# Optimization experiments

Hardware: AMD Instinct MI355X
Metric: run time of the kernel (lower is better)

Reference implementation:

```python
import jax, jax.numpy as jnp
import numpy as np

P = 16        # patch_size
SP = 8        # shift_pixels = int(patch_size * shift_ratio)
EPS = 1e-5    # torch LayerNorm default eps


def _bilinear_shift(img, sx, sy):
    """Replicates F.grid_sample(bilinear, zeros padding, align_corners=False)
    with a pure translation grid: out[y, x] = img[y + sy, x + sx] (bilinear)."""
    B, C, H, W = img.shape
    ys = jnp.arange(H, dtype=img.dtype) + jnp.asarray(sy, img.dtype)
    xs = jnp.arange(W, dtype=img.dtype) + jnp.asarray(sx, img.dtype)
    y0 = jnp.floor(ys)
    x0 = jnp.floor(xs)
    wy = ys - y0  # [H]
    wx = xs - x0  # [W]

    def gather(iy, ix):
        valid = ((iy >= 0) & (iy < H))[:, None] & ((ix >= 0) & (ix < W))[None, :]
        iyc = jnp.clip(iy, 0, H - 1).astype(jnp.int32)
        ixc = jnp.clip(ix, 0, W - 1).astype(jnp.int32)
        v = img[:, :, iyc][:, :, :, ixc]  # [B, C, H, W]
        return v * valid.astype(img.dtype)

    w00 = (1 - wy)[:, None] * (1 - wx)[None, :]
    w01 = (1 - wy)[:, None] * wx[None, :]
    w10 = wy[:, None] * (1 - wx)[None, :]
    w11 = wy[:, None] * wx[None, :]
    return (w00 * gather(y0, x0) + w01 * gather(y0, x0 + 1)
            + w10 * gather(y0 + 1, x0) + w11 * gather(y0 + 1, x0 + 1))


def reference(x, ln_gamma, ln_beta, w, b):
    B, C, H, W = x.shape
    # Original bug: shift_y = (shift_x * 2 / W) * 2 / H, so the effective
    # vertical pixel shift is ty*H/2 = 2*SP/W (sign of shift_x; dy ignored).
    ty_pix = 2.0 * SP / W
    right_up = _bilinear_shift(x, +SP, +ty_pix)
    left_up = _bilinear_shift(x, -SP, -ty_pix)
    right_down = _bilinear_shift(x, +SP, +ty_pix)
    left_down = _bilinear_shift(x, -SP, -ty_pix)
    xc = jnp.concatenate([x, left_up, right_up, left_down, right_down], axis=1)  # [B, 5C, H, W]
    C5 = xc.shape[1]
    h, ww = H // P, W // P
    # Rearrange 'B C (p1 h) (p2 w) -> B (h w) (C p1 p2)'  (p1/p2 are OUTER factors)
    p = xc.reshape(B, C5, P, h, P, ww)
    p = p.transpose(0, 3, 5, 1, 2, 4).reshape(B, h * ww, C5 * P * P)  # [B, 196, 3840]
    # LayerNorm (biased variance, as in torch)
    mu = p.mean(axis=-1, keepdims=True)
    var = p.var(axis=-1, keepdims=True)
    p = (p - mu) * jax.lax.rsqrt(var + EPS) * ln_gamma + ln_beta
    # Linear
    return p @ w + b  # [B, 196, 768]


def setup_inputs() -> dict:
    key = jax.random.key(0)
    k1, k2 = jax.random.split(key)
    d_in = P * P * 5 * 3  # 3840
    d_model = 768
    return {
        "x": jax.random.normal(k1, (64, 3, 224, 224), dtype=jnp.float32),
        "ln_gamma": jnp.ones((d_in,), dtype=jnp.float32),
        "ln_beta": jnp.zeros((d_in,), dtype=jnp.float32),
        "w": jax.random.normal(k2, (d_in, d_model), dtype=jnp.float32) / np.sqrt(d_in),
        "b": jnp.zeros((d_model,), dtype=jnp.float32),
    }
```

## Files before the change

kernel.cpp:

```cpp
#include <hip/hip_runtime.h>


typedef short bf16x8 __attribute__((ext_vector_type(8)));
typedef unsigned short u16x8 __attribute__((ext_vector_type(8)));
typedef float f32x4 __attribute__((ext_vector_type(4)));

#define GLOBAL_AS __attribute__((address_space(1)))
#define LDS_AS __attribute__((address_space(3)))

__device__ __forceinline__ unsigned short f2bf(float f) {
  union { float f; unsigned int u; } v;
  v.f = f;
  unsigned int u = v.u;
  unsigned int r = (u + 0x7FFFu + ((u >> 16) & 1u)) >> 16;
  return (unsigned short)r;
}

__global__ __launch_bounds__(256) void spt_fold_w(
    const float* __restrict__ gamma, const float* __restrict__ beta,
    const float* __restrict__ w, unsigned short* __restrict__ w2t,
    float* __restrict__ Gp, float* __restrict__ Bp)
{
  __shared__ float tile[16][257];
  const int f2blk = blockIdx.x * 16;
  const int jblk  = blockIdx.y * 256;
  const int t = threadIdx.x;
  const int j = jblk + t;
  float gacc = 0.f, bacc = 0.f;
  #pragma unroll
  for (int i = 0; i < 16; ++i) {
    const int f2 = f2blk + i;
    const int g = f2 / 768;
    const int rem = f2 % 768;
    float v, bv;
    if (g == 0) {
      const int f = rem;
      const float wv = w[(size_t)f * 768 + j];
      v = gamma[f] * wv;
      bv = beta[f] * wv;
    } else if (g == 1) {
      const int fa = 768 + rem, fb = 2304 + rem;
      const float wa = w[(size_t)fa * 768 + j], wb = w[(size_t)fb * 768 + j];
      v = gamma[fa] * wa + gamma[fb] * wb;
      bv = beta[fa] * wa + beta[fb] * wb;
    } else {
      const int fa = 1536 + rem, fb = 3072 + rem;
      const float wa = w[(size_t)fa * 768 + j], wb = w[(size_t)fb * 768 + j];
      v = gamma[fa] * wa + gamma[fb] * wb;
      bv = beta[fa] * wa + beta[fb] * wb;
    }
    tile[i][t] = v;
    gacc += v;
    bacc += bv;
  }
  __syncthreads();
  u16x8 lo, hi;
  #pragma unroll
  for (int i = 0; i < 8; ++i) {
    lo[i] = f2bf(tile[i][t]);
    hi[i] = f2bf(tile[8 + i][t]);
  }
  unsigned short* dst = w2t + (size_t)j * 2304 + f2blk;
  *(u16x8*)dst = lo;
  *(u16x8*)(dst + 8) = hi;
  Gp[blockIdx.x * 768 + j] = gacc;
  Bp[blockIdx.x * 768 + j] = bacc;
}

__global__ __launch_bounds__(256) void spt_gb(
    const float* __restrict__ Gp, const float* __restrict__ Bp,
    const float* __restrict__ bvec, float* __restrict__ G, float* __restrict__ Bt)
{
  const int j = blockIdx.x * 256 + threadIdx.x;
  float g = 0.f, bb = 0.f;
  for (int i = 0; i < 144; ++i) {
    g += Gp[i * 768 + j];
    bb += Bp[i * 768 + j];
  }
  G[j] = g;
  Bt[j] = bb + bvec[j];
}

__global__ __launch_bounds__(256) void spt_pack(
    const float* __restrict__ x, unsigned short* __restrict__ V,
    float2* __restrict__ stats)
{
  __shared__ unsigned short slab[14 * 2312];
  __shared__ float sred[4][224];
  __shared__ float qred[4][224];
  const int bi = blockIdx.x;
  const int b = bi / 14, hi = bi % 14;
  const int t = threadIdx.x;
  const float TW = 16.0f / 224.0f;

  const int q = t % 56;
  const int grp = t / 56;
  const int x4 = q * 4;

  int sloff[4];
  {
    int wi = x4 % 14, p2 = x4 / 14;
    #pragma unroll
    for (int j = 0; j < 4; ++j) {
      sloff[j] = wi * 2312 + p2;
      if (++wi == 14) { wi = 0; ++p2; }
    }
  }

  if (t < 224) {
    f32x4 sAcc = {0.f, 0.f, 0.f, 0.f}, qAcc = {0.f, 0.f, 0.f, 0.f};
    #pragma unroll
    for (int it = 0; it < 12; ++it) {
      const int cp = grp * 12 + it;
      const int c = cp >> 4, p1 = cp & 15;
      const int y = p1 * 14 + hi;
      const float* row = x + ((size_t)(b * 3 + c)) * 50176 + (size_t)y * 224;
      const f32x4 xv = *(const f32x4*)(row + x4);
      f32x4 ra = {0.f,0.f,0.f,0.f}, rb = {0.f,0.f,0.f,0.f};
      f32x4 la = {0.f,0.f,0.f,0.f}, lb = {0.f,0.f,0.f,0.f};
      if (q < 54) {
        ra = *(const f32x4*)(row + x4 + 8);
        if (y < 223) rb = *(const f32x4*)(row + x4 + 8 + 224);
      }
      if (q >= 2) {
        la = *(const f32x4*)(row + x4 - 8);
        if (y > 0) lb = *(const f32x4*)(row + x4 - 8 - 224);
      }
      const f32x4 rv = (1.0f - TW) * ra + TW * rb;
      const f32x4 lv = (1.0f - TW) * la + TW * lb;
      sAcc += xv + 2.0f * (lv + rv);
      qAcc += xv * xv + 2.0f * (lv * lv + rv * rv);
      const int kb = c * 256 + p1 * 16;
      #pragma unroll
      for (int j = 0; j < 4; ++j) {
        slab[sloff[j] + kb]        = f2bf(xv[j]);
        slab[sloff[j] + kb + 768]  = f2bf(lv[j]);
        slab[sloff[j] + kb + 1536] = f2bf(rv[j]);
      }
    }
    #pragma unroll
    for (int j = 0; j < 4; ++j) {
      sred[grp][x4 + j] = sAcc[j];
      qred[grp][x4 + j] = qAcc[j];
    }
  }
  __syncthreads();

  float ss = 0.f, qq = 0.f;
  if (t < 224) {
    ss = sred[0][t] + sred[1][t] + sred[2][t] + sred[3][t];
    qq = qred[0][t] + qred[1][t] + qred[2][t] + qred[3][t];
  }
  __syncthreads();
  if (t < 224) { sred[0][t] = ss; qred[0][t] = qq; }
  __syncthreads();

  const int tok0 = b * 196 + hi * 14;
  if (t < 14) {
    float S = 0.f, Q = 0.f;
    #pragma unroll
    for (int p = 0; p < 16; ++p) { S += sred[0][t + 14 * p]; Q += qred[0][t + 14 * p]; }
    const float mu = S / 3840.f;
    const float var = Q / 3840.f - mu * mu;
    const float r = rsqrtf(var + 1e-5f);
    stats[tok0 + t] = make_float2(r, -mu * r);
  }

  if (t < 224) {
    const int wi2 = t >> 4, sub = t & 15;
    const size_t vbase = (size_t)(tok0 + wi2) * 2304;
    #pragma unroll
    for (int cc = 0; cc < 18; ++cc) {
      const int off8 = (cc * 16 + sub) * 8;
      *(u16x8*)&V[vbase + off8] = *(const u16x8*)&slab[wi2 * 2312 + off8];
    }
  }
}

__global__ __launch_bounds__(256, 2) void spt_gemm(
    const unsigned short* __restrict__ V, const unsigned short* __restrict__ w2t,
    const float2* __restrict__ stats, const float* __restrict__ G,
    const float* __restrict__ Bt, float* __restrict__ out)
{
  __shared__ unsigned short Alds[2][224 * 64];
  __shared__ unsigned short Blds[2][96 * 64];

  const int orig = blockIdx.x;
  const int wgid = (orig & 7) * 56 + (orig >> 3);
  const int m0 = (wgid >> 3) * 224;
  const int n0 = (wgid & 7) * 96;
  const int t = threadIdx.x;
  const int w = t >> 6, l = t & 63;
  const int wr = w >> 1;
  const int wn = w & 1;

  f32x4 acc[7][3] = {};

#define STAGE(pb, kt)                                                          \
  {                                                                            \
    const int k0s = (kt) << 6;                                                 \
    _Pragma("unroll") for (int i = 0; i < 7; ++i) {                            \
      const int c = i * 256 + t;                                               \
      const int row = c >> 3;                                                  \
      const int srcel = (((c & 7) ^ (row & 7)) << 3);                          \
      const unsigned short* ga = V + (size_t)(m0 + row) * 2304 + k0s + srcel;  \
      __builtin_amdgcn_global_load_lds((const GLOBAL_AS unsigned int*)ga,      \
          (LDS_AS unsigned int*)&Alds[pb][i * 2048 + w * 512], 16, 0, 0);      \
    }                                                                          \
    _Pragma("unroll") for (int i = 0; i < 3; ++i) {                            \
      const int c = i * 256 + t;                                               \
      const int row = c >> 3;                                                  \
      const int srcel = (((c & 7) ^ (row & 7)) << 3);                          \
      const unsigned short* gb = w2t + (size_t)(n0 + row) * 2304 + k0s + srcel;\
      __builtin_amdgcn_global_load_lds((const GLOBAL_AS unsigned int*)gb,      \
          (LDS_AS unsigned int*)&Blds[pb][i * 2048 + w * 512], 16, 0, 0);      \
    }                                                                          \
  }

#define COMPUTE(pb)                                                            \
  {                                                                            \
    const int lane15 = l & 15;                                                 \
    const int kcol = (l >> 4) << 4;                                            \
    _Pragma("unroll") for (int kk = 0; kk < 2; ++kk) {                         \
      const int kb = kk * 64 + kcol;                                           \
      bf16x8 bF[3];                                                            \
      _Pragma("unroll") for (int n = 0; n < 3; ++n) {                          \
        const int row = wn * 48 + n * 16 + lane15;                             \
        const int phys = row * 128 + (kb ^ ((row & 7) << 4));                  \
        bF[n] = *(const bf16x8*)&Blds[pb][phys >> 1];                          \
      }                                                                        \
      _Pragma("unroll") for (int m = 0; m < 7; ++m) {                          \
        const int row = wr * 112 + m * 16 + lane15;                            \
        const int phys = row * 128 + (kb ^ ((row & 7) << 4));                  \
        const bf16x8 aF = *(const bf16x8*)&Alds[pb][phys >> 1];                \
        _Pragma("unroll") for (int n = 0; n < 3; ++n)                          \
          acc[m][n] = __builtin_amdgcn_mfma_f32_16x16x32_bf16(aF, bF[n],       \
                                                              acc[m][n], 0, 0, 0); \
      }                                                                        \
    }                                                                          \
  }

  STAGE(0, 0);
  int pb = 0;
  for (int kt = 0; kt < 35; ++kt) {
    STAGE(pb ^ 1, kt + 1);
    asm volatile("s_waitcnt vmcnt(10)\n\ts_barrier" ::: "memory");
    COMPUTE(pb);
    asm volatile("s_barrier" ::: "memory");
    pb ^= 1;
  }
  asm volatile("s_waitcnt vmcnt(0)\n\ts_barrier" ::: "memory");
  COMPUTE(pb);

  const int lane15 = l & 15;
  const int lg = (l >> 4) * 4;
  #pragma unroll
  for (int m = 0; m < 7; ++m) {
    const int rowb = m0 + wr * 112 + m * 16 + lg;
    float2 st[4];
    #pragma unroll
    for (int r = 0; r < 4; ++r) st[r] = stats[rowb + r];
    #pragma unroll
    for (int n = 0; n < 3; ++n) {
      const int col = n0 + wn * 48 + n * 16 + lane15;
      const float Gc = G[col];
      const float Bc = Bt[col];
      #pragma unroll
      for (int r = 0; r < 4; ++r) {
        out[(size_t)(rowb + r) * 768 + col] = st[r].x * acc[m][n][r] + st[r].y * Gc + Bc;
      }
    }
  }
#undef STAGE
#undef COMPUTE
}

extern "C" void kernel_launch(void* const* d_in, const int* in_sizes, int n_in,
                              void* d_out, int out_size, void* d_ws, size_t ws_size,
                              hipStream_t stream) {
  const float* x     = (const float*)d_in[0];
  const float* gamma = (const float*)d_in[1];
  const float* beta  = (const float*)d_in[2];
  const float* w     = (const float*)d_in[3];
  const float* bvec  = (const float*)d_in[4];
  float* out = (float*)d_out;

  char* ws = (char*)d_ws;
  unsigned short* V   = (unsigned short*)(ws);
  unsigned short* w2t = (unsigned short*)(ws + 57802752);
  float2* stats       = (float2*)(ws + 61341696);
  float* G            = (float*)(ws + 61442048);
  float* Bt           = (float*)(ws + 61445120);
  float* Gp           = (float*)(ws + 61448192);
  float* Bp           = (float*)(ws + 61890560);

  spt_pack<<<896, 256, 0, stream>>>(x, V, stats);
  spt_fold_w<<<dim3(144, 3), 256, 0, stream>>>(gamma, beta, w, w2t, Gp, Bp);
  spt_gb<<<3, 256, 0, stream>>>(Gp, Bp, bvec, G, Bt);
  spt_gemm<<<448, 256, 0, stream>>>(V, w2t, stats, G, Bt, out);
}
```

Measured before the change: 101.4 us.

## Widen GEMM tile to 224x192 with 8 waves and warp-specialized staging

After: 109.0 us. 7.4% more time.

```diff
diff --git a/kernel.cpp b/kernel.cpp
--- a/kernel.cpp
+++ b/kernel.cpp
@@ -177,80 +177,88 @@
   }
 }
 
-__global__ __launch_bounds__(256, 2) void spt_gemm(
+__global__ __launch_bounds__(512, 1) void spt_gemm(
     const unsigned short* __restrict__ V, const unsigned short* __restrict__ w2t,
     const float2* __restrict__ stats, const float* __restrict__ G,
     const float* __restrict__ Bt, float* __restrict__ out)
 {
   __shared__ unsigned short Alds[2][224 * 64];
-  __shared__ unsigned short Blds[2][96 * 64];
+  __shared__ unsigned short Blds[2][192 * 64];
 
   const int orig = blockIdx.x;
-  const int wgid = (orig & 7) * 56 + (orig >> 3);
-  const int m0 = (wgid >> 3) * 224;
-  const int n0 = (wgid & 7) * 96;
+  const int wgid = (orig & 7) * 28 + (orig >> 3);
+  const int m0 = (wgid >> 2) * 224;
+  const int n0 = (wgid & 3) * 192;
   const int t = threadIdx.x;
   const int w = t >> 6, l = t & 63;
-  const int wr = w >> 1;
-  const int wn = w & 1;
+  const int wr = w >> 2;
+  const int wn = w & 3;
 
   f32x4 acc[7][3] = {};
 
 #define STAGE(pb, kt)                                                          \
   {                                                                            \
     const int k0s = (kt) << 6;                                                 \
-    _Pragma("unroll") for (int i = 0; i < 7; ++i) {                            \
-      const int c = i * 256 + t;                                               \
-      const int row = c >> 3;                                                  \
-      const int srcel = (((c & 7) ^ (row & 7)) << 3);                          \
-      const unsigned short* ga = V + (size_t)(m0 + row) * 2304 + k0s + srcel;  \
-      __builtin_amdgcn_global_load_lds((const GLOBAL_AS unsigned int*)ga,      \
-          (LDS_AS unsigned int*)&Alds[pb][i * 2048 + w * 512], 16, 0, 0);      \
+    const int srcel = (((l & 7) ^ (l >> 3)) << 3);                             \
+    if (w < 4) {                                                               \
+      _Pragma("unroll") for (int i = 0; i < 7; ++i) {                          \
+        const int base = w * 7 + i;                                            \
+        const int row = base * 8 + (l >> 3);                                   \
+        const unsigned short* ga = V + (size_t)(m0 + row) * 2304 + k0s + srcel;\
+        __builtin_amdgcn_global_load_lds((const GLOBAL_AS unsigned int*)ga,    \
+            (LDS_AS unsigned int*)&Alds[pb][base * 512], 16, 0, 0);            \
+      }                                                                        \
+    } else {                                                                   \
+      _Pragma("unroll") for (int i = 0; i < 6; ++i) {                          \
+        const int base = (w - 4) * 6 + i;                                      \
+        const int row = base * 8 + (l >> 3);                                   \
+        const unsigned short* gb = w2t + (size_t)(n0 + row) * 2304 + k0s + srcel;\
+        __builtin_amdgcn_global_load_lds((const GLOBAL_AS unsigned int*)gb,    \
+            (LDS_AS unsigned int*)&Blds[pb][base * 512], 16, 0, 0);            \
+      }                                                                        \
     }                                                                          \
-    _Pragma("unroll") for (int i = 0; i < 3; ++i) {                            \
-      const int c = i * 256 + t;                                               \
-      const int row = c >> 3;                                                  \
-      const int srcel = (((c & 7) ^ (row & 7)) << 3);                          \
-      const unsigned short* gb = w2t + (size_t)(n0 + row) * 2304 + k0s + srcel;\
-      __builtin_amdgcn_global_load_lds((const GLOBAL_AS unsigned int*)gb,      \
-          (LDS_AS unsigned int*)&Blds[pb][i * 2048 + w * 512], 16, 0, 0);      \
-    }                                                                          \
-  }
-
-#define COMPUTE(pb)                                                            \
+  }
+
+#define PHASE(pb, kk)                                                          \
   {                                                                            \
     const int lane15 = l & 15;                                                 \
-    const int kcol = (l >> 4) << 4;                                            \
-    _Pragma("unroll") for (int kk = 0; kk < 2; ++kk) {                         \
-      const int kb = kk * 64 + kcol;                                           \
-      bf16x8 bF[3];                                                            \
-      _Pragma("unroll") for (int n = 0; n < 3; ++n) {                          \
-        const int row = wn * 48 + n * 16 + lane15;                             \
-        const int phys = row * 128 + (kb ^ ((row & 7) << 4));                  \
-        bF[n] = *(const bf16x8*)&Blds[pb][phys >> 1];                          \
-      }                                                                        \
-      _Pragma("unroll") for (int m = 0; m < 7; ++m) {                          \
-        const int row = wr * 112 + m * 16 + lane15;                            \
-        const int phys = row * 128 + (kb ^ ((row & 7) << 4));                  \
-        const bf16x8 aF = *(const bf16x8*)&Alds[pb][phys >> 1];                \
-        _Pragma("unroll") for (int n = 0; n < 3; ++n)                          \
-          acc[m][n] = __builtin_amdgcn_mfma_f32_16x16x32_bf16(aF, bF[n],       \
-                                                              acc[m][n], 0, 0, 0); \
-      }                                                                        \
+    const int kb = (kk) * 64 + ((l >> 4) << 4);                                \
+    bf16x8 aF[7], bF[3];                                                       \
+    _Pragma("unroll") for (int n = 0; n < 3; ++n) {                            \
+      const int row = wn * 48 + n * 16 + lane15;                               \
+      const int phys = row * 128 + (kb ^ ((row & 7) << 4));                    \
+      bF[n] = *(const bf16x8*)&Blds[pb][phys >> 1];                            \
     }                                                                          \
+    _Pragma("unroll") for (int m = 0; m < 7; ++m) {                            \
+      const int row = wr * 112 + m * 16 + lane15;                              \
+      const int phys = row * 128 + (kb ^ ((row & 7) << 4));                    \
+      aF[m] = *(const bf16x8*)&Alds[pb][phys >> 1];                            \
+    }                                                                          \
+    asm volatile("s_barrier" ::: "memory");                                    \
+    __builtin_amdgcn_s_setprio(1);                                             \
+    _Pragma("unroll") for (int m = 0; m < 7; ++m)                              \
+      _Pragma("unroll") for (int n = 0; n < 3; ++n)                            \
+        acc[m][n] = __builtin_amdgcn_mfma_f32_16x16x32_bf16(aF[m], bF[n],      \
+                                                            acc[m][n], 0, 0, 0); \
+    __builtin_amdgcn_s_setprio(0);                                             \
+    asm volatile("s_barrier" ::: "memory");                                    \
   }
 
   STAGE(0, 0);
-  int pb = 0;
+  STAGE(1, 1);
   for (int kt = 0; kt < 35; ++kt) {
-    STAGE(pb ^ 1, kt + 1);
-    asm volatile("s_waitcnt vmcnt(10)\n\ts_barrier" ::: "memory");
-    COMPUTE(pb);
+    const int pb = kt & 1;
+    if (w < 4) asm volatile("s_waitcnt vmcnt(7)" ::: "memory");
+    else       asm volatile("s_waitcnt vmcnt(6)" ::: "memory");
     asm volatile("s_barrier" ::: "memory");
-    pb ^= 1;
-  }
-  asm volatile("s_waitcnt vmcnt(0)\n\ts_barrier" ::: "memory");
-  COMPUTE(pb);
+    PHASE(pb, 0);
+    PHASE(pb, 1);
+    if (kt < 34) STAGE(pb, kt + 2);
+  }
+  asm volatile("s_waitcnt vmcnt(0)" ::: "memory");
+  asm volatile("s_barrier" ::: "memory");
+  PHASE(1, 0);
+  PHASE(1, 1);
 
   const int lane15 = l & 15;
   const int lg = (l >> 4) * 4;
@@ -272,7 +280,7 @@
     }
   }
 #undef STAGE
-#undef COMPUTE
+#undef PHASE
 }
 
 extern "C" void kernel_launch(void* const* d_in, const int* in_sizes, int n_in,
@@ -297,5 +305,5 @@
   spt_pack<<<896, 256, 0, stream>>>(x, V, stats);
   spt_fold_w<<<dim3(144, 3), 256, 0, stream>>>(gamma, beta, w, w2t, Gp, Bp);
   spt_gb<<<3, 256, 0, stream>>>(Gp, Bp, bvec, G, Bt);
-  spt_gemm<<<448, 256, 0, stream>>>(V, w2t, stats, G, Bt, out);
-}
+  spt_gemm<<<224, 512, 0, stream>>>(V, w2t, stats, G, Bt, out);
+}
```

## Widen GEMM tile to 224x192 with register double-buffered LDS fragment reads

Applied to the files above, without the earlier changes.

New measurement: 127.9 us. 1.26x slower.

```diff
diff --git a/kernel.cpp b/kernel.cpp
--- a/kernel.cpp
+++ b/kernel.cpp
@@ -177,24 +177,25 @@
   }
 }
 
-__global__ __launch_bounds__(256, 2) void spt_gemm(
+__global__ __launch_bounds__(256, 1) void spt_gemm(
     const unsigned short* __restrict__ V, const unsigned short* __restrict__ w2t,
     const float2* __restrict__ stats, const float* __restrict__ G,
     const float* __restrict__ Bt, float* __restrict__ out)
 {
   __shared__ unsigned short Alds[2][224 * 64];
-  __shared__ unsigned short Blds[2][96 * 64];
+  __shared__ unsigned short Blds[2][192 * 64];
 
   const int orig = blockIdx.x;
-  const int wgid = (orig & 7) * 56 + (orig >> 3);
-  const int m0 = (wgid >> 3) * 224;
-  const int n0 = (wgid & 7) * 96;
+  const int wgid = (orig & 7) * 28 + (orig >> 3);
+  const int m0 = (wgid >> 2) * 224;
+  const int n0 = (wgid & 3) * 192;
   const int t = threadIdx.x;
   const int w = t >> 6, l = t & 63;
   const int wr = w >> 1;
   const int wn = w & 1;
 
-  f32x4 acc[7][3] = {};
+  f32x4 acc[7][6] = {};
+  bf16x8 fXA[7], fXB[6], fYA[7], fYB[6];
 
 #define STAGE(pb, kt)                                                          \
   {                                                                            \
@@ -205,52 +206,55 @@
       const int srcel = (((c & 7) ^ (row & 7)) << 3);                          \
       const unsigned short* ga = V + (size_t)(m0 + row) * 2304 + k0s + srcel;  \
       __builtin_amdgcn_global_load_lds((const GLOBAL_AS unsigned int*)ga,      \
-          (LDS_AS unsigned int*)&Alds[pb][i * 2048 + w * 512], 16, 0, 0);      \
+          (LDS_AS unsigned int*)&Alds[pb][c * 8], 16, 0, 0);                   \
     }                                                                          \
-    _Pragma("unroll") for (int i = 0; i < 3; ++i) {                            \
+    _Pragma("unroll") for (int i = 0; i < 6; ++i) {                            \
       const int c = i * 256 + t;                                               \
       const int row = c >> 3;                                                  \
       const int srcel = (((c & 7) ^ (row & 7)) << 3);                          \
       const unsigned short* gb = w2t + (size_t)(n0 + row) * 2304 + k0s + srcel;\
       __builtin_amdgcn_global_load_lds((const GLOBAL_AS unsigned int*)gb,      \
-          (LDS_AS unsigned int*)&Blds[pb][i * 2048 + w * 512], 16, 0, 0);      \
+          (LDS_AS unsigned int*)&Blds[pb][c * 8], 16, 0, 0);                   \
     }                                                                          \
   }
 
-#define COMPUTE(pb)                                                            \
+#define READF(FA, FB, pb, kkb)                                                 \
   {                                                                            \
     const int lane15 = l & 15;                                                 \
-    const int kcol = (l >> 4) << 4;                                            \
-    _Pragma("unroll") for (int kk = 0; kk < 2; ++kk) {                         \
-      const int kb = kk * 64 + kcol;                                           \
-      bf16x8 bF[3];                                                            \
-      _Pragma("unroll") for (int n = 0; n < 3; ++n) {                          \
-        const int row = wn * 48 + n * 16 + lane15;                             \
-        const int phys = row * 128 + (kb ^ ((row & 7) << 4));                  \
-        bF[n] = *(const bf16x8*)&Blds[pb][phys >> 1];                          \
-      }                                                                        \
-      _Pragma("unroll") for (int m = 0; m < 7; ++m) {                          \
-        const int row = wr * 112 + m * 16 + lane15;                            \
-        const int phys = row * 128 + (kb ^ ((row & 7) << 4));                  \
-        const bf16x8 aF = *(const bf16x8*)&Alds[pb][phys >> 1];                \
-        _Pragma("unroll") for (int n = 0; n < 3; ++n)                          \
-          acc[m][n] = __builtin_amdgcn_mfma_f32_16x16x32_bf16(aF, bF[n],       \
-                                                              acc[m][n], 0, 0, 0); \
-      }                                                                        \
+    const int kb = (kkb) + ((l >> 4) << 4);                                    \
+    _Pragma("unroll") for (int n = 0; n < 6; ++n) {                            \
+      const int row = wn * 96 + n * 16 + lane15;                               \
+      const int phys = row * 128 + (kb ^ ((row & 7) << 4));                    \
+      FB[n] = *(const bf16x8*)&Blds[pb][phys >> 1];                            \
     }                                                                          \
-  }
+    _Pragma("unroll") for (int m = 0; m < 7; ++m) {                            \
+      const int row = wr * 112 + m * 16 + lane15;                              \
+      const int phys = row * 128 + (kb ^ ((row & 7) << 4));                    \
+      FA[m] = *(const bf16x8*)&Alds[pb][phys >> 1];                            \
+    }                                                                          \
+  }
+
+#define MF(FA, FB)                                                             \
+  _Pragma("unroll") for (int m = 0; m < 7; ++m)                                \
+    _Pragma("unroll") for (int n = 0; n < 6; ++n)                              \
+      acc[m][n] = __builtin_amdgcn_mfma_f32_16x16x32_bf16(FA[m], FB[n],        \
+                                                          acc[m][n], 0, 0, 0);
 
   STAGE(0, 0);
-  int pb = 0;
-  for (int kt = 0; kt < 35; ++kt) {
-    STAGE(pb ^ 1, kt + 1);
-    asm volatile("s_waitcnt vmcnt(10)\n\ts_barrier" ::: "memory");
-    COMPUTE(pb);
-    asm volatile("s_barrier" ::: "memory");
-    pb ^= 1;
-  }
-  asm volatile("s_waitcnt vmcnt(0)\n\ts_barrier" ::: "memory");
-  COMPUTE(pb);
+  STAGE(1, 1);
+  asm volatile("s_waitcnt vmcnt(13)" ::: "memory");
+  asm volatile("s_barrier" ::: "memory");
+  READF(fXA, fXB, 0, 0);
+
+  for (int kt = 0; kt < 36; ++kt) {
+    const int pb = kt & 1;
+    READF(fYA, fYB, pb, 64);
+    MF(fXA, fXB);
+    asm volatile("s_waitcnt lgkmcnt(0) vmcnt(0)\n\ts_barrier" ::: "memory");
+    if (kt < 34) STAGE(pb, kt + 2);
+    if (kt < 35) READF(fXA, fXB, pb ^ 1, 0);
+    MF(fYA, fYB);
+  }
 
   const int lane15 = l & 15;
   const int lg = (l >> 4) * 4;
@@ -261,8 +265,8 @@
     #pragma unroll
     for (int r = 0; r < 4; ++r) st[r] = stats[rowb + r];
     #pragma unroll
-    for (int n = 0; n < 3; ++n) {
-      const int col = n0 + wn * 48 + n * 16 + lane15;
+    for (int n = 0; n < 6; ++n) {
+      const int col = n0 + wn * 96 + n * 16 + lane15;
       const float Gc = G[col];
       const float Bc = Bt[col];
       #pragma unroll
@@ -272,7 +276,8 @@
     }
   }
 #undef STAGE
-#undef COMPUTE
+#undef READF
+#undef MF
 }
 
 extern "C" void kernel_launch(void* const* d_in, const int* in_sizes, int n_in,
@@ -297,5 +302,5 @@
   spt_pack<<<896, 256, 0, stream>>>(x, V, stats);
   spt_fold_w<<<dim3(144, 3), 256, 0, stream>>>(gamma, beta, w, w2t, Gp, Bp);
   spt_gb<<<3, 256, 0, stream>>>(Gp, Bp, bvec, G, Bt);
-  spt_gemm<<<448, 256, 0, stream>>>(V, w2t, stats, G, Bt, out);
-}
+  spt_gemm<<<224, 256, 0, stream>>>(V, w2t, stats, G, Bt, out);
+}
```
